# Performance work log

Measured on AMD Instinct MI355X. Metric: run time of the kernel, lower is better.

Reference implementation:

```python
import jax, jax.numpy as jnp
import numpy as np

B, S, D, H = 2, 512, 1024, 8
DK = D // H
DFF = 4 * D
R = 51
SEP = 64


def setup_inputs() -> dict:
    key = jax.random.key(0)
    ks = jax.random.split(key, 12)
    def w(k, shape, scale=0.02):
        return jax.random.normal(k, shape, jnp.float32) * scale
    return {
        "x": jax.random.normal(ks[0], (B, S, D), jnp.float32),
        "relation": jax.random.randint(ks[1], (B, S, S), 0, R),
        "mask": jnp.ones((B, S, S), jnp.int32),
        "sep_id": SEP,
        "history_reg": jnp.ones((1,), jnp.float32),
        "Wq": w(ks[2], (D, D)), "bq": jnp.zeros((D,), jnp.float32),
        "Wk": w(ks[3], (D, D)), "bk": jnp.zeros((D,), jnp.float32),
        "Wv": w(ks[4], (D, D)), "bv": jnp.zeros((D,), jnp.float32),
        "Wo": w(ks[5], (D, D)), "bo": jnp.zeros((D,), jnp.float32),
        "rel_k_emb": w(ks[6], (R, DK)),
        "rel_v_emb": w(ks[7], (R, DK)),
        "ln1_g": jnp.ones((D,), jnp.float32), "ln1_b": jnp.zeros((D,), jnp.float32),
        "ln2_g": jnp.ones((D,), jnp.float32), "ln2_b": jnp.zeros((D,), jnp.float32),
        "W1": w(ks[8], (D, DFF)), "b1": jnp.zeros((DFF,), jnp.float32),
        "W2": w(ks[9], (DFF, D)), "b2": jnp.zeros((D,), jnp.float32),
    }


def _layer_norm(x, g, b, eps=1e-5):
    m = jnp.mean(x, axis=-1, keepdims=True)
    v = jnp.mean(jnp.square(x - m), axis=-1, keepdims=True)
    return (x - m) * jax.lax.rsqrt(v + eps) * g + b


def _forward(x, relation, mask, sep_id, history_reg, Wq, bq, Wk, bk, Wv, bv, Wo, bo,
             rel_k_emb, rel_v_emb, ln1_g, ln1_b, ln2_g, ln2_b, W1, b1, W2, b2):
    b, s, d = x.shape
    # relation-aware self-attention sublayer (pre-norm)
    h = _layer_norm(x, ln1_g, ln1_b)
    rk = rel_k_emb[relation]  # [B,S,S,DK]
    rv = rel_v_emb[relation]  # [B,S,S,DK]
    def proj(W, bias):
        return (h @ W + bias).reshape(b, s, H, DK).transpose(0, 2, 1, 3)  # [B,H,S,DK]
    q, k, v = proj(Wq, bq), proj(Wk, bk), proj(Wv, bv)
    scores = jnp.einsum("bhid,bhjd->bhij", q, k) + jnp.einsum("bhid,bijd->bhij", q, rk)
    scores = scores / jnp.sqrt(jnp.float32(DK))
    scores = jnp.where(mask[:, None, :, :] == 0, jnp.float32(-1e9), scores)
    attn = jax.nn.softmax(scores, axis=-1)  # [B,H,S,S]
    ctx = jnp.einsum("bhij,bhjd->bhid", attn, v) + jnp.einsum("bhij,bijd->bhid", attn, rv)
    ctx = ctx.transpose(0, 2, 1, 3).reshape(b, s, d)
    attn_out = ctx @ Wo + bo
    # history regularization loss: attention mass on history tokens (positions < sep_id)
    loss = history_reg[0] * jnp.mean(attn[:, :, :, :sep_id])
    x = x + attn_out
    # FFN sublayer (pre-norm)
    h2 = _layer_norm(x, ln2_g, ln2_b)
    ffn = jax.nn.relu(h2 @ W1 + b1) @ W2 + b2
    x = x + ffn
    return x, loss


def reference(x, relation, mask, sep_id, history_reg, Wq, bq, Wk, bk, Wv, bv, Wo, bo,
              rel_k_emb, rel_v_emb, ln1_g, ln1_b, ln2_g, ln2_b, W1, b1, W2, b2):
    return _forward(x, relation, mask, sep_id, history_reg, Wq, bq, Wk, bk, Wv, bv,
                    Wo, bo, rel_k_emb, rel_v_emb, ln1_g, ln1_b, ln2_g, ln2_b,
                    W1, b1, W2, b2)
```

## Files before the change

kernel.cpp:

```cpp
#include <hip/hip_runtime.h>
#include <hip/hip_bf16.h>

#define NB 2
#define NS 512
#define ND 1024
#define NH 8
#define NDK 128
#define NDFF 4096
#define RPAD 64
#define BSROWS 1024
#define NBH 16
#define QT 8
#define SLB 536

typedef __bf16 bf16x8 __attribute__((ext_vector_type(8)));
typedef __bf16 bf16x4 __attribute__((ext_vector_type(4)));
typedef float f32x4 __attribute__((ext_vector_type(4)));

#define BM 64
#define BN 64
#define BK 64

__device__ __forceinline__ void gload16(const void* g, void* l) {
    __builtin_amdgcn_global_load_lds(
        (const __attribute__((address_space(1))) void*)g,
        (__attribute__((address_space(3))) void*)l, 16, 0, 0);
}

__global__ __launch_bounds__(256, 4) void gemm64(
    const __bf16* __restrict__ A, const __bf16* __restrict__ Bt,
    __bf16* __restrict__ vt,
    float* __restrict__ Cf, __bf16* __restrict__ Cb,
    const float* __restrict__ bias,
    int Ksp, int lda, int ldb, int ldc,
    long sA, long sA2, int zdivA,
    long sB, long sB2, int zdivB,
    long sC, int nsplit, long sPart, int flags)
{
    __shared__ __bf16 As0[BM * BK];
    __shared__ __bf16 As1[BM * BK];
    __shared__ __bf16 Bs0[BN * BK];
    __shared__ __bf16 Bs1[BN * BK];

    const unsigned gx = gridDim.x, gy = gridDim.y;
    const unsigned n = gx * gy * gridDim.z;
    const unsigned o = blockIdx.x + gx * (blockIdx.y + gy * blockIdx.z);
    const unsigned q = n >> 3, r = n & 7, xcd = o & 7;
    const unsigned nl = (xcd < r ? xcd * (q + 1) : r * (q + 1) + (xcd - r) * q) + (o >> 3);
    const unsigned bx = nl % gx, tmp = nl / gx;
    const unsigned by = tmp % gy, bz = tmp / gy;

    const int z = bz;
    const int bh = z / nsplit, sp = z - bh * nsplit;
    const long kbase = (long)sp * Ksp;
    A  += (long)(bh / zdivA) * sA + (long)(bh % zdivA) * sA2 + kbase;
    Bt += (long)(bh / zdivB) * sB + (long)(bh % zdivB) * sB2 + kbase;
    const long cbase = (long)bh * sC + (long)sp * sPart;

    const int tM = by * BM, tN = bx * BN;
    const int t = threadIdx.x, lane = t & 63, w = t >> 6;
    const int wr = w >> 1, wc = w & 1;

    const int srow = lane >> 3;
    const int scolE = ((((lane & 7) << 4) ^ (srow << 4)) >> 1);

    const __bf16* gA = A + (long)(tM + srow) * lda + scolE;
    const __bf16* gB = Bt + (long)(tN + srow) * ldb + scolE;

    f32x4 acc[2][2];
#pragma unroll
    for (int m = 0; m < 2; ++m)
#pragma unroll
        for (int nn = 0; nn < 2; ++nn)
#pragma unroll
            for (int j = 0; j < 4; ++j) acc[m][nn][j] = 0.f;

    const int r16 = lane & 15;
    const int kq = (lane >> 4) * 8;
    const int xorE = (r16 & 7) * 8;
    const int nt = Ksp / BK;

    auto STAGE = [&](__bf16* as, __bf16* bs, int k0) {
#pragma unroll
        for (int i = 0; i < 2; ++i) {
            const int rr = (w + i * 4) * 8;
            gload16(gA + (long)rr * lda + k0, (void*)&as[rr * BK]);
            gload16(gB + (long)rr * ldb + k0, (void*)&bs[rr * BK]);
        }
    };
    auto COMPUTE = [&](const __bf16* as, const __bf16* bs) {
        __builtin_amdgcn_s_setprio(1);
#pragma unroll
        for (int ks = 0; ks < 2; ++ks) {
            bf16x8 af[2], bv[2];
#pragma unroll
            for (int m = 0; m < 2; ++m)
                af[m] = *(const bf16x8*)&as[(wr * 32 + m * 16 + r16) * BK + ((ks * 32 + kq) ^ xorE)];
#pragma unroll
            for (int nn = 0; nn < 2; ++nn)
                bv[nn] = *(const bf16x8*)&bs[(wc * 32 + nn * 16 + r16) * BK + ((ks * 32 + kq) ^ xorE)];
#pragma unroll
            for (int m = 0; m < 2; ++m)
#pragma unroll
                for (int nn = 0; nn < 2; ++nn)
                    acc[m][nn] = __builtin_amdgcn_mfma_f32_16x16x32_bf16(af[m], bv[nn], acc[m][nn], 0, 0, 0);
        }
        __builtin_amdgcn_s_setprio(0);
    };

    STAGE(As0, Bs0, 0);
    STAGE(As1, Bs1, BK);
    for (int tt = 0; tt < nt; tt += 2) {
        asm volatile("s_waitcnt vmcnt(4)\n\ts_barrier" ::: "memory");
        COMPUTE(As0, Bs0);
        asm volatile("s_waitcnt lgkmcnt(0)\n\ts_barrier" ::: "memory");
        const bool more = (tt + 2 < nt);
        if (more) {
            STAGE(As0, Bs0, (tt + 2) * BK);
            asm volatile("s_waitcnt vmcnt(4)\n\ts_barrier" ::: "memory");
        } else {
            asm volatile("s_waitcnt vmcnt(0)\n\ts_barrier" ::: "memory");
        }
        COMPUTE(As1, Bs1);
        asm volatile("s_waitcnt lgkmcnt(0)\n\ts_barrier" ::: "memory");
        if (more) STAGE(As1, Bs1, (tt + 3) * BK);
    }

    const bool relu = (flags & 1) != 0;
    const bool vmode = (flags & 8) && (tN >= 2 * ND);
#pragma unroll
    for (int m = 0; m < 2; ++m) {
        const int gr0 = tM + wr * 32 + m * 16 + (lane >> 4) * 4;
#pragma unroll
        for (int nn = 0; nn < 2; ++nn) {
            const int gc = tN + wc * 32 + nn * 16 + (lane & 15);
            const float bb = bias ? bias[gc] : 0.f;
            if (vmode) {
                const int hd = gc - 2 * ND;
                const int b = gr0 >> 9, i = gr0 & 511;
                bf16x4 ov;
#pragma unroll
                for (int j = 0; j < 4; ++j) ov[j] = (__bf16)(acc[m][nn][j] + bb);
                *(bf16x4*)&vt[(((long)b * NH + (hd >> 7)) * NDK + (hd & 127)) * NS + i] = ov;
            } else {
#pragma unroll
                for (int j = 0; j < 4; ++j) {
                    float v = acc[m][nn][j] + bb;
                    if (relu) v = fmaxf(v, 0.f);
                    const long idx = cbase + (long)(gr0 + j) * ldc + gc;
                    if (Cb) Cb[idx] = (__bf16)v;
                    else Cf[idx] = v;
                }
            }
        }
    }
}

__global__ __launch_bounds__(256, 4) void attn_fused(
    const __bf16* __restrict__ qkvb, const __bf16* __restrict__ vt,
    const __bf16* __restrict__ relkT, const __bf16* __restrict__ relvT,
    const int* __restrict__ relation, const int* __restrict__ mask,
    __bf16* __restrict__ ctxm, float* __restrict__ loss_part,
    const int* __restrict__ sep_p)
{
    __shared__ __bf16 Sl[QT * SLB];
    __shared__ __bf16 Ks[64 * NDK];
    __shared__ float qrl[QT][RPAD];
    __shared__ float bins[QT][68];
    __shared__ float redl[4];

    const unsigned o = blockIdx.x + 64u * blockIdx.y;
    const unsigned nl = (o & 7) * 128u + (o >> 3);
    const int qt = nl & 63, bh = nl >> 6;
    const int b = bh >> 3, h = bh & 7;
    const int i0 = qt * QT;

    const int t = threadIdx.x, lane = t & 63, w = t >> 6;
    const int r16 = lane & 15;
    const int r8 = r16 & 7;
    const int kq = (lane >> 4) * 8;
    const int xorE = r8 * 8;
    const int sep = *sep_p;

    bf16x8 qf[4];
    {
        const __bf16* qrow = qkvb + ((long)(b * NS + i0 + r8)) * (3 * ND) + h * NDK;
#pragma unroll
        for (int ks = 0; ks < 4; ++ks)
            qf[ks] = *(const bf16x8*)(qrow + ks * 32 + kq);
    }

    int4 ra[2][2], ma[2][2];
#pragma unroll
    for (int rr = 0; rr < 2; ++rr) {
        const long rg = (long)(b * NS + i0 + w * 2 + rr) * NS;
        ra[rr][0] = ((const int4*)(relation + rg))[lane * 2];
        ra[rr][1] = ((const int4*)(relation + rg))[lane * 2 + 1];
        ma[rr][0] = ((const int4*)(mask + rg))[lane * 2];
        ma[rr][1] = ((const int4*)(mask + rg))[lane * 2 + 1];
    }

    const int brow = t & 7;
    const int bj0 = (t >> 3) * 16;
    int4 br[4];
    {
        const int4* rp = (const int4*)(relation + ((long)(b * NS + i0 + brow)) * NS + bj0);
#pragma unroll
        for (int c = 0; c < 4; ++c) br[c] = rp[c];
    }

    {
        f32x4 a;
#pragma unroll
        for (int j = 0; j < 4; ++j) a[j] = 0.f;
#pragma unroll
        for (int ks = 0; ks < 4; ++ks) {
            const bf16x8 bfr = *(const bf16x8*)(relkT + (long)(w * 16 + r16) * NDK + ks * 32 + kq);
            a = __builtin_amdgcn_mfma_f32_16x16x32_bf16(qf[ks], bfr, a, 0, 0, 0);
        }
#pragma unroll
        for (int j = 0; j < 4; ++j) {
            const int row = (lane >> 4) * 4 + j;
            if (row < QT) qrl[row][w * 16 + (lane & 15)] = a[j];
        }
    }
    for (int idx = t; idx < QT * 68; idx += 256) ((float*)bins)[idx] = 0.f;

    auto KSTAGE = [&](int kv0) {
#pragma unroll
        for (int ii = 0; ii < 4; ++ii) {
            const int Lc = (w * 4 + ii) * 64 + lane;
            const int j = Lc >> 4, cc = Lc & 15;
            gload16(qkvb + ((long)(b * NS + kv0 + j)) * (3 * ND) + ND + h * NDK + ((cc ^ (j & 7)) << 3),
                    (void*)&Ks[(w * 4 + ii) * 512]);
        }
    };
    auto SCOMP = [&](int kv0) {
        f32x4 s;
#pragma unroll
        for (int j = 0; j < 4; ++j) s[j] = 0.f;
#pragma unroll
        for (int ks = 0; ks < 4; ++ks) {
            const bf16x8 bfr = *(const bf16x8*)&Ks[(w * 16 + r16) * NDK + ((ks * 32 + kq) ^ xorE)];
            s = __builtin_amdgcn_mfma_f32_16x16x32_bf16(qf[ks], bfr, s, 0, 0, 0);
        }
        const int colb = kv0 + w * 16 + (lane & 15);
#pragma unroll
        for (int j = 0; j < 4; ++j) {
            const int row = (lane >> 4) * 4 + j;
            if (row < QT) Sl[row * SLB + colb] = (__bf16)s[j];
        }
    };

    for (int tt = 0; tt < 8; ++tt) {
        KSTAGE(tt * 64);
        asm volatile("s_waitcnt vmcnt(0)\n\ts_barrier" ::: "memory");
        SCOMP(tt * 64);
        asm volatile("s_waitcnt lgkmcnt(0)\n\ts_barrier" ::: "memory");
    }

    const float sc = 0.088388347648318447f;
    float lsum = 0.f;
#pragma unroll
    for (int rr = 0; rr < 2; ++rr) {
        const int row = w * 2 + rr;
        const bf16x8 sv = *(const bf16x8*)&Sl[row * SLB + lane * 8];
        int rl[8], mm[8];
        rl[0] = ra[rr][0].x; rl[1] = ra[rr][0].y; rl[2] = ra[rr][0].z; rl[3] = ra[rr][0].w;
        rl[4] = ra[rr][1].x; rl[5] = ra[rr][1].y; rl[6] = ra[rr][1].z; rl[7] = ra[rr][1].w;
        mm[0] = ma[rr][0].x; mm[1] = ma[rr][0].y; mm[2] = ma[rr][0].z; mm[3] = ma[rr][0].w;
        mm[4] = ma[rr][1].x; mm[5] = ma[rr][1].y; mm[6] = ma[rr][1].z; mm[7] = ma[rr][1].w;
        float v[8];
        float mx = -1e30f;
#pragma unroll
        for (int q = 0; q < 8; ++q) {
            float vv = ((float)sv[q] + qrl[row][rl[q]]) * sc;
            if (mm[q] == 0) vv = -1e9f;
            v[q] = vv;
            mx = fmaxf(mx, vv);
        }
#pragma unroll
        for (int of = 32; of > 0; of >>= 1) mx = fmaxf(mx, __shfl_xor(mx, of, 64));
        float sm = 0.f;
#pragma unroll
        for (int q = 0; q < 8; ++q) { v[q] = __expf(v[q] - mx); sm += v[q]; }
#pragma unroll
        for (int of = 32; of > 0; of >>= 1) sm += __shfl_xor(sm, of, 64);
        const float inv = 1.f / sm;
        bf16x8 av;
#pragma unroll
        for (int q = 0; q < 8; ++q) {
            const float a = v[q] * inv;
            av[q] = (__bf16)a;
            if (lane * 8 + q < sep) lsum += a;
        }
        *(bf16x8*)&Sl[row * SLB + lane * 8] = av;
    }
#pragma unroll
    for (int of = 32; of > 0; of >>= 1) lsum += __shfl_xor(lsum, of, 64);
    if (lane == 0) redl[w] = lsum;
    asm volatile("s_waitcnt lgkmcnt(0)\n\ts_barrier" ::: "memory");
    if (t == 0) loss_part[bh * 64 + qt] = redl[0] + redl[1] + redl[2] + redl[3];

    {
        const __bf16* ap = &Sl[brow * SLB + bj0];
#pragma unroll
        for (int c = 0; c < 4; ++c) {
            const bf16x4 a4 = *(const bf16x4*)(ap + c * 4);
            atomicAdd(&bins[brow][br[c].x], (float)a4[0]);
            atomicAdd(&bins[brow][br[c].y], (float)a4[1]);
            atomicAdd(&bins[brow][br[c].z], (float)a4[2]);
            atomicAdd(&bins[brow][br[c].w], (float)a4[3]);
        }
    }

    f32x4 oacc[2];
#pragma unroll
    for (int nn = 0; nn < 2; ++nn)
#pragma unroll
        for (int j = 0; j < 4; ++j) oacc[nn][j] = 0.f;

    auto VSTAGE = [&](int kv0) {
#pragma unroll
        for (int ii = 0; ii < 4; ++ii) {
            const int d = w * 32 + ii * 8 + (lane >> 3);
            const int cc = lane & 7;
            gload16(vt + ((long)bh * NDK + d) * NS + kv0 + ((cc ^ (d & 7)) << 3),
                    (void*)&Ks[(w * 32 + ii * 8) * 64]);
        }
    };
    auto PVCOMP = [&](int kv0) {
        __builtin_amdgcn_s_setprio(1);
#pragma unroll
        for (int ks = 0; ks < 2; ++ks) {
            const bf16x8 af = *(const bf16x8*)&Sl[r8 * SLB + kv0 + ks * 32 + kq];
#pragma unroll
            for (int nn = 0; nn < 2; ++nn) {
                const bf16x8 bv = *(const bf16x8*)&Ks[(w * 32 + nn * 16 + r16) * 64 + ((ks * 32 + kq) ^ xorE)];
                oacc[nn] = __builtin_amdgcn_mfma_f32_16x16x32_bf16(af, bv, oacc[nn], 0, 0, 0);
            }
        }
        __builtin_amdgcn_s_setprio(0);
    };

    for (int tt = 0; tt < 8; ++tt) {
        VSTAGE(tt * 64);
        asm volatile("s_waitcnt vmcnt(0)\n\ts_barrier" ::: "memory");
        PVCOMP(tt * 64);
        asm volatile("s_waitcnt lgkmcnt(0)\n\ts_barrier" ::: "memory");
    }

#pragma unroll
    for (int kc = 0; kc < 2; ++kc) {
        const float4 b0 = *(const float4*)&bins[r8][kc * 32 + kq];
        const float4 b1 = *(const float4*)&bins[r8][kc * 32 + kq + 4];
        bf16x8 af;
        af[0] = (__bf16)b0.x; af[1] = (__bf16)b0.y; af[2] = (__bf16)b0.z; af[3] = (__bf16)b0.w;
        af[4] = (__bf16)b1.x; af[5] = (__bf16)b1.y; af[6] = (__bf16)b1.z; af[7] = (__bf16)b1.w;
#pragma unroll
        for (int nn = 0; nn < 2; ++nn) {
            const bf16x8 bfr = *(const bf16x8*)(relvT + (long)(w * 32 + nn * 16 + r16) * RPAD + kc * 32 + kq);
            oacc[nn] = __builtin_amdgcn_mfma_f32_16x16x32_bf16(af, bfr, oacc[nn], 0, 0, 0);
        }
    }
#pragma unroll
    for (int nn = 0; nn < 2; ++nn)
#pragma unroll
        for (int j = 0; j < 4; ++j) {
            const int row = (lane >> 4) * 4 + j;
            if (row < QT)
                ctxm[((long)(b * NS + i0 + row)) * ND + h * NDK + w * 32 + nn * 16 + (lane & 15)] =
                    (__bf16)oacc[nn][j];
        }
}

__global__ void prep_weights(
    const float* __restrict__ Wq, const float* __restrict__ Wk,
    const float* __restrict__ Wv, const float* __restrict__ Wo,
    const float* __restrict__ W1, const float* __restrict__ W2,
    const float* __restrict__ relv,
    const float* __restrict__ bq, const float* __restrict__ bk,
    const float* __restrict__ bv, const float* __restrict__ relk,
    const float* __restrict__ x, const float* __restrict__ ln1g,
    const float* __restrict__ ln1b,
    __bf16* __restrict__ WqkvT, __bf16* __restrict__ WoT,
    __bf16* __restrict__ W1T, __bf16* __restrict__ W2T,
    __bf16* __restrict__ relvT, float* __restrict__ biasqkv,
    __bf16* __restrict__ relkT, __bf16* __restrict__ h1, int R)
{
    const int tile = blockIdx.x;
    const int t = threadIdx.y * 32 + threadIdx.x;

    if (tile >= 12372) {
        const long row = tile - 12372;
        const float* xr = x + row * ND;
        float4 v = reinterpret_cast<const float4*>(xr)[t];
        float s = v.x + v.y + v.z + v.w;
        float s2 = v.x * v.x + v.y * v.y + v.z * v.z + v.w * v.w;
#pragma unroll
        for (int o = 32; o > 0; o >>= 1) {
            s += __shfl_xor(s, o, 64);
            s2 += __shfl_xor(s2, o, 64);
        }
        __shared__ float red[8];
        const int lane = t & 63, wv = t >> 6;
        if (lane == 0) { red[wv] = s; red[4 + wv] = s2; }
        __syncthreads();
        s = red[0] + red[1] + red[2] + red[3];
        s2 = red[4] + red[5] + red[6] + red[7];
        const float mean = s * (1.f / ND);
        const float var = s2 * (1.f / ND) - mean * mean;
        const float rs = rsqrtf(var + 1e-5f);
        const float xv[4] = {v.x, v.y, v.z, v.w};
        bf16x4 o;
#pragma unroll
        for (int j = 0; j < 4; ++j) {
            const int c = t * 4 + j;
            o[j] = (__bf16)((xv[j] - mean) * rs * ln1g[c] + ln1b[c]);
        }
        *(bf16x4*)&h1[row * ND + t * 4] = o;
        return;
    }
    if (tile >= 12296) {
        const int ft = (tile - 12296) * 256 + t;
        if (ft < ND) biasqkv[ft] = bq[ft];
        else if (ft < 2 * ND) biasqkv[ft] = bk[ft - ND];
        else if (ft < 3 * ND) biasqkv[ft] = bv[ft - 2 * ND];
        else {
            const int idx = ft - 3 * ND;
            if (idx < 128 * NDK) {
                const int r = idx / NDK;
                relkT[idx] = (r < R) ? (__bf16)relk[idx] : (__bf16)0.f;
            }
        }
        return;
    }
    const float* src; __bf16* dst;
    int rows_in, cols_in, ldo, kx, ny;
    if (tile < 4096) {
        const int m = tile >> 10, r = tile & 1023;
        kx = r & 31; ny = r >> 5;
        rows_in = 1024; cols_in = 1024; ldo = 1024;
        src = m == 0 ? Wq : m == 1 ? Wk : m == 2 ? Wv : Wo;
        dst = m == 3 ? WoT : WqkvT + (size_t)m * 1024 * 1024;
    } else if (tile < 8192) {
        const int r = tile - 4096;
        kx = r & 31; ny = r >> 5;
        rows_in = 1024; cols_in = 4096; ldo = 1024; src = W1; dst = W1T;
    } else if (tile < 12288) {
        const int r = tile - 8192;
        kx = r & 127; ny = r >> 7;
        rows_in = 4096; cols_in = 1024; ldo = 4096; src = W2; dst = W2T;
    } else {
        const int r = tile - 12288;
        kx = r & 1; ny = r >> 1;
        rows_in = R; cols_in = 128; ldo = 64; src = relv; dst = relvT;
    }

    __shared__ float tl[32][33];
    const int k0 = kx * 32, n0 = ny * 32;
    const int tx = threadIdx.x, ty = threadIdx.y;
#pragma unroll
    for (int dy = 0; dy < 32; dy += 8) {
        const int k = k0 + ty + dy, nn = n0 + tx;
        tl[ty + dy][tx] = (k < rows_in && nn < cols_in) ? src[(long)k * cols_in + nn] : 0.f;
    }
    __syncthreads();
#pragma unroll
    for (int dy = 0; dy < 32; dy += 8) {
        const int nn = n0 + ty + dy, k = k0 + tx;
        if (nn < cols_in && k < ldo) dst[(long)nn * ldo + k] = (__bf16)tl[tx][ty + dy];
    }
}

__global__ __launch_bounds__(256) void wo_reduce_ln(
    const float* __restrict__ P, const float* __restrict__ x,
    const float* __restrict__ bo, const float* __restrict__ g,
    const float* __restrict__ bb, float* __restrict__ out,
    __bf16* __restrict__ h2)
{
    const int row = blockIdx.x;
    const int t = threadIdx.x;
    const long i4 = (long)row * 256 + t;
    const long sP = (long)BSROWS * ND / 4;
    const float4* P4 = (const float4*)P;
    float4 s = P4[i4];
    const float4 t1 = P4[i4 + sP];
    s.x += t1.x; s.y += t1.y; s.z += t1.z; s.w += t1.w;
    const int col = t * 4;
    const float4 xv = ((const float4*)x)[i4];
    const float4 bv = *(const float4*)&bo[col];
    float4 o;
    o.x = s.x + xv.x + bv.x; o.y = s.y + xv.y + bv.y;
    o.z = s.z + xv.z + bv.z; o.w = s.w + xv.w + bv.w;
    ((float4*)out)[i4] = o;

    float sum = o.x + o.y + o.z + o.w;
    float sum2 = o.x * o.x + o.y * o.y + o.z * o.z + o.w * o.w;
#pragma unroll
    for (int of = 32; of > 0; of >>= 1) {
        sum += __shfl_xor(sum, of, 64);
        sum2 += __shfl_xor(sum2, of, 64);
    }
    __shared__ float red[8];
    const int lane = t & 63, wv = t >> 6;
    if (lane == 0) { red[wv] = sum; red[4 + wv] = sum2; }
    __syncthreads();
    sum = red[0] + red[1] + red[2] + red[3];
    sum2 = red[4] + red[5] + red[6] + red[7];
    const float mean = sum * (1.f / ND);
    const float var = sum2 * (1.f / ND) - mean * mean;
    const float rs = rsqrtf(var + 1e-5f);
    const float ov[4] = {o.x, o.y, o.z, o.w};
    bf16x4 hb;
#pragma unroll
    for (int j = 0; j < 4; ++j)
        hb[j] = (__bf16)((ov[j] - mean) * rs * g[col + j] + bb[col + j]);
    *(bf16x4*)&h2[(long)row * ND + col] = hb;
}

__global__ __launch_bounds__(256) void ffn2_reduce(
    const float* __restrict__ P, const float* __restrict__ b2, float* __restrict__ out,
    const float* __restrict__ loss_part, const float* __restrict__ hist,
    const int* __restrict__ sep_p, float* __restrict__ out_loss)
{
    const int i4 = blockIdx.x * 256 + threadIdx.x;
    const long sP = (long)BSROWS * ND / 4;
    const float4* P4 = (const float4*)P;
    float4 s = P4[i4];
    const float4 t1 = P4[i4 + sP];
    s.x += t1.x; s.y += t1.y; s.z += t1.z; s.w += t1.w;
    const int col = (i4 * 4) & (ND - 1);
    const float4 bv = *(const float4*)&b2[col];
    float4 o = ((float4*)out)[i4];
    o.x += s.x + bv.x; o.y += s.y + bv.y;
    o.z += s.z + bv.z; o.w += s.w + bv.w;
    ((float4*)out)[i4] = o;

    if (blockIdx.x == 0) {
        const int t = threadIdx.x;
        const float4 v = ((const float4*)loss_part)[t];
        float ls = v.x + v.y + v.z + v.w;
#pragma unroll
        for (int of = 32; of > 0; of >>= 1) ls += __shfl_xor(ls, of, 64);
        __shared__ float red[4];
        if ((t & 63) == 0) red[t >> 6] = ls;
        __syncthreads();
        if (t == 0) {
            const int sep = *sep_p;
            const float total = red[0] + red[1] + red[2] + red[3];
            const float denom = (float)NB * NH * NS * (float)(sep > 0 ? sep : 1);
            out_loss[0] = (sep > 0) ? hist[0] * total / denom : 0.f;
        }
    }
}

extern "C" void kernel_launch(void* const* d_in, const int* in_sizes, int n_in,
                              void* d_out, int out_size, void* d_ws, size_t ws_size,
                              hipStream_t stream)
{
    const float* x      = (const float*)d_in[0];
    const int* relation = (const int*)d_in[1];
    const int* mask     = (const int*)d_in[2];
    const int* sep_p    = (const int*)d_in[3];
    const float* hist   = (const float*)d_in[4];
    const float* Wq = (const float*)d_in[5],  *bq = (const float*)d_in[6];
    const float* Wk = (const float*)d_in[7],  *bk = (const float*)d_in[8];
    const float* Wv = (const float*)d_in[9],  *bv = (const float*)d_in[10];
    const float* Wo = (const float*)d_in[11], *bo = (const float*)d_in[12];
    const float* relk = (const float*)d_in[13];
    const float* relv = (const float*)d_in[14];
    const float* ln1g = (const float*)d_in[15], *ln1b = (const float*)d_in[16];
    const float* ln2g = (const float*)d_in[17], *ln2b = (const float*)d_in[18];
    const float* W1 = (const float*)d_in[19], *b1 = (const float*)d_in[20];
    const float* W2 = (const float*)d_in[21], *b2 = (const float*)d_in[22];
    const int R = in_sizes[13] / NDK;

    float* out = (float*)d_out;
    float* out_loss = out + (long)BSROWS * ND;

    char* p = (char*)d_ws;
    auto alloc = [&](size_t bytes) -> void* {
        void* r = (void*)p;
        p += (bytes + 255) & ~(size_t)255;
        return r;
    };
    __bf16* WqkvT   = (__bf16*)alloc((size_t)3 * ND * ND * 2);
    __bf16* WoT     = (__bf16*)alloc((size_t)ND * ND * 2);
    __bf16* W1T     = (__bf16*)alloc((size_t)NDFF * ND * 2);
    __bf16* W2T     = (__bf16*)alloc((size_t)ND * NDFF * 2);
    __bf16* relkT   = (__bf16*)alloc((size_t)128 * NDK * 2);
    __bf16* relvT   = (__bf16*)alloc((size_t)NDK * RPAD * 2);
    float*  biasqkv = (float*)alloc((size_t)3 * ND * 4);
    __bf16* h1      = (__bf16*)alloc((size_t)BSROWS * ND * 2);
    __bf16* qkvb    = (__bf16*)alloc((size_t)BSROWS * 3 * ND * 2);
    __bf16* vt      = (__bf16*)alloc((size_t)NBH * NDK * NS * 2);
    __bf16* ctxm    = (__bf16*)alloc((size_t)BSROWS * ND * 2);
    __bf16* h2      = (__bf16*)alloc((size_t)BSROWS * ND * 2);
    __bf16* F1      = (__bf16*)alloc((size_t)BSROWS * NDFF * 2);
    float*  loss_part = (float*)alloc((size_t)1024 * 4);
    float*  arena   = (float*)alloc((size_t)16 * 1024 * 1024);
    float* woPart   = arena;
    float* f2Part   = arena + (size_t)2 * 1024 * 1024;

    const dim3 tb(32, 8);
    prep_weights<<<13396, tb, 0, stream>>>(Wq, Wk, Wv, Wo, W1, W2, relv,
                                           bq, bk, bv, relk, x, ln1g, ln1b,
                                           WqkvT, WoT, W1T, W2T, relvT,
                                           biasqkv, relkT, h1, R);

    gemm64<<<dim3(48, 16, 1), 256, 0, stream>>>(
        h1, WqkvT, vt, nullptr, qkvb, biasqkv,
        ND, ND, ND, 3 * ND,
        0, 0, 1, 0, 0, 1, 0, 1, 0, 8);

    attn_fused<<<dim3(64, 16), 256, 0, stream>>>(
        qkvb, vt, relkT, relvT, relation, mask, ctxm, loss_part, sep_p);

    gemm64<<<dim3(16, 16, 2), 256, 0, stream>>>(
        ctxm, WoT, nullptr, woPart, nullptr, nullptr,
        512, ND, ND, ND,
        0, 0, 1, 0, 0, 1,
        0, 2, (long)BSROWS * ND, 0);

    wo_reduce_ln<<<BSROWS, 256, 0, stream>>>(woPart, x, bo, ln2g, ln2b, out, h2);

    gemm64<<<dim3(64, 16, 1), 256, 0, stream>>>(
        h2, W1T, nullptr, nullptr, F1, b1,
        ND, ND, ND, NDFF,
        0, 0, 1, 0, 0, 1, 0, 1, 0, 1);

    gemm64<<<dim3(16, 16, 2), 256, 0, stream>>>(
        F1, W2T, nullptr, f2Part, nullptr, nullptr,
        2048, NDFF, NDFF, ND,
        0, 0, 1, 0, 0, 1,
        0, 2, (long)BSROWS * ND, 0);

    ffn2_reduce<<<1024, 256, 0, stream>>>(f2Part, b2, out,
                                          loss_part, hist, sep_p, out_loss);
}
```

Baseline: 136.6 us.

## Load K and V fragments directly from global memory in attention kernel

Removes the LDS staging of K and V tiles in the fused attention kernel. Each wave now reads its MFMA B-operand fragments straight from global memory, with the tile loops fully unrolled. This drops the 16 KB Ks buffer and the per-tile barriers, which can raise occupancy and lets loads be issued early. In exchange, each K/V element is read from global memory (via L2) by the waves that use it rather than once into shared memory, and the accesses are less coalesced.

```diff
diff --git a/kernel.cpp b/kernel.cpp
--- a/kernel.cpp
+++ b/kernel.cpp
@@ -164,7 +164,6 @@
     const int* __restrict__ sep_p)
 {
     __shared__ __bf16 Sl[QT * SLB];
-    __shared__ __bf16 Ks[64 * NDK];
     __shared__ float qrl[QT][RPAD];
     __shared__ float bins[QT][68];
     __shared__ float redl[4];
@@ -179,7 +178,6 @@
     const int r16 = lane & 15;
     const int r8 = r16 & 7;
     const int kq = (lane >> 4) * 8;
-    const int xorE = r8 * 8;
     const int sep = *sep_p;
 
     bf16x8 qf[4];
@@ -226,38 +224,28 @@
     }
     for (int idx = t; idx < QT * 68; idx += 256) ((float*)bins)[idx] = 0.f;
 
-    auto KSTAGE = [&](int kv0) {
-#pragma unroll
-        for (int ii = 0; ii < 4; ++ii) {
-            const int Lc = (w * 4 + ii) * 64 + lane;
-            const int j = Lc >> 4, cc = Lc & 15;
-            gload16(qkvb + ((long)(b * NS + kv0 + j)) * (3 * ND) + ND + h * NDK + ((cc ^ (j & 7)) << 3),
-                    (void*)&Ks[(w * 4 + ii) * 512]);
-        }
-    };
-    auto SCOMP = [&](int kv0) {
-        f32x4 s;
-#pragma unroll
-        for (int j = 0; j < 4; ++j) s[j] = 0.f;
-#pragma unroll
-        for (int ks = 0; ks < 4; ++ks) {
-            const bf16x8 bfr = *(const bf16x8*)&Ks[(w * 16 + r16) * NDK + ((ks * 32 + kq) ^ xorE)];
-            s = __builtin_amdgcn_mfma_f32_16x16x32_bf16(qf[ks], bfr, s, 0, 0, 0);
-        }
-        const int colb = kv0 + w * 16 + (lane & 15);
-#pragma unroll
-        for (int j = 0; j < 4; ++j) {
-            const int row = (lane >> 4) * 4 + j;
-            if (row < QT) Sl[row * SLB + colb] = (__bf16)s[j];
-        }
-    };
-
-    for (int tt = 0; tt < 8; ++tt) {
-        KSTAGE(tt * 64);
-        asm volatile("s_waitcnt vmcnt(0)\n\ts_barrier" ::: "memory");
-        SCOMP(tt * 64);
-        asm volatile("s_waitcnt lgkmcnt(0)\n\ts_barrier" ::: "memory");
-    }
+    {
+        const __bf16* kb = qkvb + ((long)(b * NS + w * 16 + r16)) * (3 * ND) + ND + h * NDK;
+#pragma unroll
+        for (int tt = 0; tt < 8; ++tt) {
+            const __bf16* krow = kb + (long)(tt * 64) * (3 * ND);
+            f32x4 s;
+#pragma unroll
+            for (int j = 0; j < 4; ++j) s[j] = 0.f;
+#pragma unroll
+            for (int ks = 0; ks < 4; ++ks) {
+                const bf16x8 bfr = *(const bf16x8*)(krow + ks * 32 + kq);
+                s = __builtin_amdgcn_mfma_f32_16x16x32_bf16(qf[ks], bfr, s, 0, 0, 0);
+            }
+            const int colb = tt * 64 + w * 16 + (lane & 15);
+#pragma unroll
+            for (int j = 0; j < 4; ++j) {
+                const int row = (lane >> 4) * 4 + j;
+                if (row < QT) Sl[row * SLB + colb] = (__bf16)s[j];
+            }
+        }
+    }
+    __syncthreads();
 
     const float sc = 0.088388347648318447f;
     float lsum = 0.f;
@@ -299,7 +287,7 @@
 #pragma unroll
     for (int of = 32; of > 0; of >>= 1) lsum += __shfl_xor(lsum, of, 64);
     if (lane == 0) redl[w] = lsum;
-    asm volatile("s_waitcnt lgkmcnt(0)\n\ts_barrier" ::: "memory");
+    __syncthreads();
     if (t == 0) loss_part[bh * 64 + qt] = redl[0] + redl[1] + redl[2] + redl[3];
 
     {
@@ -320,35 +308,22 @@
 #pragma unroll
         for (int j = 0; j < 4; ++j) oacc[nn][j] = 0.f;
 
-    auto VSTAGE = [&](int kv0) {
-#pragma unroll
-        for (int ii = 0; ii < 4; ++ii) {
-            const int d = w * 32 + ii * 8 + (lane >> 3);
-            const int cc = lane & 7;
-            gload16(vt + ((long)bh * NDK + d) * NS + kv0 + ((cc ^ (d & 7)) << 3),
-                    (void*)&Ks[(w * 32 + ii * 8) * 64]);
-        }
-    };
-    auto PVCOMP = [&](int kv0) {
-        __builtin_amdgcn_s_setprio(1);
-#pragma unroll
-        for (int ks = 0; ks < 2; ++ks) {
-            const bf16x8 af = *(const bf16x8*)&Sl[r8 * SLB + kv0 + ks * 32 + kq];
-#pragma unroll
-            for (int nn = 0; nn < 2; ++nn) {
-                const bf16x8 bv = *(const bf16x8*)&Ks[(w * 32 + nn * 16 + r16) * 64 + ((ks * 32 + kq) ^ xorE)];
-                oacc[nn] = __builtin_amdgcn_mfma_f32_16x16x32_bf16(af, bv, oacc[nn], 0, 0, 0);
+    {
+        const __bf16* vb = vt + ((long)bh * NDK + w * 32 + r16) * NS;
+#pragma unroll
+        for (int tt = 0; tt < 8; ++tt) {
+#pragma unroll
+            for (int ks = 0; ks < 2; ++ks) {
+                const bf16x8 af = *(const bf16x8*)&Sl[r8 * SLB + tt * 64 + ks * 32 + kq];
+#pragma unroll
+                for (int nn = 0; nn < 2; ++nn) {
+                    const bf16x8 bv = *(const bf16x8*)(vb + (long)(nn * 16) * NS + tt * 64 + ks * 32 + kq);
+                    oacc[nn] = __builtin_amdgcn_mfma_f32_16x16x32_bf16(af, bv, oacc[nn], 0, 0, 0);
+                }
             }
         }
-        __builtin_amdgcn_s_setprio(0);
-    };
-
-    for (int tt = 0; tt < 8; ++tt) {
-        VSTAGE(tt * 64);
-        asm volatile("s_waitcnt vmcnt(0)\n\ts_barrier" ::: "memory");
-        PVCOMP(tt * 64);
-        asm volatile("s_waitcnt lgkmcnt(0)\n\ts_barrier" ::: "memory");
-    }
+    }
+    __syncthreads();
 
 #pragma unroll
     for (int kc = 0; kc < 2; ++kc) {
```

New measurement: 140.0 us. +2.5%, slower.
